# Kernel optimization log

Hardware: AMD Instinct MI355X
Metric: run time of the kernel (lower is better)

The kernel has to match this reference:

```python
import jax, jax.numpy as jnp
import numpy as np

EPS = 1e-5
NUM_HEADS = 16
HEAD_DIM = 128


def setup_inputs() -> dict:
    key = jax.random.key(0)
    ks = jax.random.split(key, 9)
    B, S, D = 2, 2048, 2048
    Hd2 = HEAD_DIM // 2
    # rotary angles: proper cos/sin of random phases (unit-modulus freqs_cis)
    theta = jax.random.uniform(ks[1], (B, S, Hd2), jnp.float32, 0.0, 2 * np.pi)
    return {
        "hidden_states": jax.random.normal(ks[0], (B, S, D), jnp.float32),
        "freqs_cos": jnp.cos(theta),
        "freqs_sin": jnp.sin(theta),
        "Wq": jax.random.normal(ks[2], (D, D), jnp.float32) * (D ** -0.5),
        "Wk": jax.random.normal(ks[3], (D, D), jnp.float32) * (D ** -0.5),
        "Wv": jax.random.normal(ks[4], (D, D), jnp.float32) * (D ** -0.5),
        "Wo": jax.random.normal(ks[5], (D, D), jnp.float32) * (D ** -0.5),
        "gq": jnp.ones((HEAD_DIM,), jnp.float32),
        "gk": jnp.ones((HEAD_DIM,), jnp.float32),
    }


def _rmsnorm(x, g):
    # normalize over last (head) dim, eps=1e-5, learned scale
    var = jnp.mean(jnp.square(x), axis=-1, keepdims=True)
    return x * jax.lax.rsqrt(var + EPS) * g


def _rope(x, cos, sin):
    # x: [B,S,H,hd]; treat last dim as hd/2 complex pairs; cos/sin: [B,S,hd/2]
    B, S, H, hd = x.shape
    xp = x.reshape(B, S, H, hd // 2, 2)
    xr, xi = xp[..., 0], xp[..., 1]
    c = cos[:, :, None, :]
    s = sin[:, :, None, :]
    out_r = xr * c - xi * s
    out_i = xr * s + xi * c
    return jnp.stack([out_r, out_i], axis=-1).reshape(B, S, H, hd)


def reference(hidden_states, freqs_cos, freqs_sin, Wq, Wk, Wv, Wo, gq, gk):
    B, S, D = hidden_states.shape
    H, hd = NUM_HEADS, HEAD_DIM
    q = (hidden_states @ Wq).reshape(B, S, H, hd)
    k = (hidden_states @ Wk).reshape(B, S, H, hd)
    v = (hidden_states @ Wv).reshape(B, S, H, hd)
    q = _rmsnorm(q, gq)
    k = _rmsnorm(k, gk)
    q = _rope(q, freqs_cos, freqs_sin)
    k = _rope(k, freqs_cos, freqs_sin)
    scale = 1.0 / np.sqrt(hd)
    scores = jnp.einsum("bqhd,bkhd->bhqk", q, k) * scale
    attn = jax.nn.softmax(scores, axis=-1)
    out = jnp.einsum("bhqk,bkhd->bqhd", attn, v)  # [B,S,H,hd]
    out = out.reshape(B, S, H * hd)
    return out @ Wo
```

## Files before the change

### kernel.cpp

```cpp
#include <hip/hip_runtime.h>
#include <hip/hip_bf16.h>

typedef __attribute__((ext_vector_type(8))) short bf16x8;
typedef __attribute__((ext_vector_type(4))) short bf16x4;
typedef __attribute__((ext_vector_type(4))) float f32x4;
typedef __attribute__((ext_vector_type(4))) int   i32x4;
typedef __attribute__((ext_vector_type(2))) unsigned u32x2;

#define D_MODEL 2048
#define NTOK    4096
#define NH      16
#define HD      128
#define SEQ     2048
#define NQKV    6144

__device__ __forceinline__ short f2bf(float f) {
  unsigned u = __builtin_bit_cast(unsigned, f);
  unsigned r = u + 0x7FFFu + ((u >> 16) & 1u);
  return (short)(r >> 16);
}
__device__ __forceinline__ float bf2f(short s) {
  return __builtin_bit_cast(float, ((unsigned)(unsigned short)s) << 16);
}

__device__ __forceinline__ float exp2fast(float x) {
#if __has_builtin(__builtin_amdgcn_exp2f)
  return __builtin_amdgcn_exp2f(x);
#else
  return exp2f(x);
#endif
}

__device__ __forceinline__ unsigned cvt_pk_bf16(float a, float b) {
  unsigned r;
  asm("v_cvt_pk_bf16_f32 %0, %1, %2" : "=v"(r) : "v"(a), "v"(b));
  return r;
}

#if __has_builtin(__builtin_amdgcn_mfma_f32_16x16x16bf16_1k)
#define MFMA16_ASM 0
__device__ __forceinline__ f32x4 mfma16(bf16x4 a, bf16x4 b, f32x4 c) {
  return __builtin_amdgcn_mfma_f32_16x16x16bf16_1k(a, b, c, 0, 0, 0);
}
#else
#define MFMA16_ASM 1
__device__ __forceinline__ f32x4 mfma16(bf16x4 a, bf16x4 b, f32x4 c) {
  asm("s_nop 3\n\tv_mfma_f32_16x16x16_bf16 %0, %1, %2, %0" : "+v"(c) : "v"(a), "v"(b));
  return c;
}
#endif

__device__ __forceinline__ void gload_lds16(const void* g, void* l) {
  typedef __attribute__((address_space(1))) const unsigned gu32;
  typedef __attribute__((address_space(3))) unsigned lu32;
  __builtin_amdgcn_global_load_lds((gu32*)(uintptr_t)g,
                                   (lu32*)(unsigned)(uintptr_t)l, 16, 0, 0);
}

__global__ __launch_bounds__(256) void cast_bf16(const float* __restrict__ in,
                                                 short* __restrict__ out, int n4) {
  int i = blockIdx.x * 256 + threadIdx.x;
  if (i >= n4) return;
  float4 v = ((const float4*)in)[i];
  short4 o;
  o.x = f2bf(v.x); o.y = f2bf(v.y); o.z = f2bf(v.z); o.w = f2bf(v.w);
  ((short4*)out)[i] = o;
}

__global__ __launch_bounds__(256) void wtrans(const float* __restrict__ w0,
                                              const float* __restrict__ w1,
                                              const float* __restrict__ w2,
                                              const float* __restrict__ w3,
                                              short* __restrict__ wt) {
  int z = blockIdx.z;
  const float* W = (z == 0) ? w0 : (z == 1) ? w1 : (z == 2) ? w2 : w3;
  short* O = wt + (size_t)z * D_MODEL * D_MODEL;
  int n0 = blockIdx.x * 64, k0 = blockIdx.y * 64;
  __shared__ short T[64 * 136];
  int tid = threadIdx.x;
#pragma unroll
  for (int it = 0; it < 4; ++it) {
    int f = it * 256 + tid, kk = f >> 4, nc = f & 15;
    float4 v = *(const float4*)&W[(size_t)(k0 + kk) * D_MODEL + n0 + nc * 4];
    short4 o;
    o.x = f2bf(v.x); o.y = f2bf(v.y); o.z = f2bf(v.z); o.w = f2bf(v.w);
    *(short4*)&T[kk * 136 + nc * 4] = o;
  }
  __syncthreads();
#pragma unroll
  for (int it = 0; it < 4; ++it) {
    int u = it * 256 + tid, nn = u >> 4, kc = u & 15;
    short4 o;
    o.x = T[(kc * 4 + 0) * 136 + nn];
    o.y = T[(kc * 4 + 1) * 136 + nn];
    o.z = T[(kc * 4 + 2) * 136 + nn];
    o.w = T[(kc * 4 + 3) * 136 + nn];
    *(short4*)&O[(size_t)(n0 + nn) * D_MODEL + k0 + kc * 4] = o;
  }
}

template <bool OUTBF16>
__global__ __launch_bounds__(512, 2) void gemm8(const short* __restrict__ A,
                                                const short* __restrict__ Bt,
                                                void* __restrict__ Cv, int CS) {
  __shared__ short L[4 * 12288];
  int tid = threadIdx.x, w = tid >> 6, lane = tid & 63, c = lane & 15, g = lane >> 4;

  int gx = gridDim.x, gy = gridDim.y;
  int lin = blockIdx.x + gx * blockIdx.y;
  int idx = lin >> 3, nst = (gx * gy) >> 7;
  int s = (lin & 7) * nst + (idx >> 4);
  int w16 = idx & 15;
  int smR = gy >> 2;
  int mblk = (s % smR) * 4 + (w16 >> 2);
  int nblk = (s / smR) * 4 + (w16 & 3);
  int m0 = mblk * 256, n0 = nblk * 128;
  int wm = w >> 1, wn = w & 1;

  const int NKT = D_MODEL / 32;

  int asrc[2], bsrc;
#pragma unroll
  for (int q = 0; q < 2; ++q) {
    int o = (2 * w + q) * 1024 + lane * 16;
    int os = o ^ (((o >> 7) & 7) << 4);
    asrc[q] = (m0 + (os >> 6)) * D_MODEL + ((os & 63) >> 1);
  }
  {
    int o = w * 1024 + lane * 16;
    int os = o ^ (((o >> 7) & 7) << 4);
    bsrc = (n0 + (os >> 6)) * D_MODEL + ((os & 63) >> 1);
  }

  int aoff[4], boff[4];
#pragma unroll
  for (int mi = 0; mi < 4; ++mi) {
    int r = wm * 64 + mi * 16 + c;
    int o = r * 64 + g * 16;
    aoff[mi] = o ^ (((o >> 7) & 7) << 4);
  }
#pragma unroll
  for (int ni = 0; ni < 4; ++ni) {
    int r = wn * 64 + ni * 16 + c;
    int o = r * 64 + g * 16;
    boff[ni] = 16384 + (o ^ (((o >> 7) & 7) << 4));
  }

  auto STAGE = [&](int jt) {
    int kk = jt * 32;
    char* base = (char*)L + (jt & 3) * 24576;
    gload_lds16(A + asrc[0] + kk, base + (2 * w) * 1024);
    gload_lds16(A + asrc[1] + kk, base + (2 * w + 1) * 1024);
    gload_lds16(Bt + bsrc + kk, base + 16384 + w * 1024);
  };

  f32x4 acc[4][4] = {};

  STAGE(0); STAGE(1); STAGE(2);
  asm volatile("s_waitcnt vmcnt(6)" ::: "memory");
  __builtin_amdgcn_s_barrier();
  asm volatile("" ::: "memory");

  for (int jt = 0; jt < NKT; ++jt) {
    if (jt + 3 < NKT) STAGE(jt + 3);
    const char* buf = (const char*)L + (jt & 3) * 24576;
    bf16x8 af[4], bfv[4];
#pragma unroll
    for (int mi = 0; mi < 4; ++mi) af[mi] = *(const bf16x8*)(buf + aoff[mi]);
#pragma unroll
    for (int ni = 0; ni < 4; ++ni) bfv[ni] = *(const bf16x8*)(buf + boff[ni]);
    __builtin_amdgcn_s_setprio(1);
#pragma unroll
    for (int mi = 0; mi < 4; ++mi)
#pragma unroll
      for (int ni = 0; ni < 4; ++ni)
        acc[mi][ni] = __builtin_amdgcn_mfma_f32_16x16x32_bf16(af[mi], bfv[ni],
                                                              acc[mi][ni], 0, 0, 0);
    __builtin_amdgcn_s_setprio(0);
    if (jt + 1 < NKT) {
      if (jt + 4 <= NKT - 1)      { asm volatile("s_waitcnt vmcnt(6)" ::: "memory"); }
      else if (jt + 3 <= NKT - 1) { asm volatile("s_waitcnt vmcnt(6)" ::: "memory"); }
      else if (jt + 2 <= NKT - 1) { asm volatile("s_waitcnt vmcnt(3)" ::: "memory"); }
      else                        { asm volatile("s_waitcnt vmcnt(0)" ::: "memory"); }
      __builtin_amdgcn_s_barrier();
      asm volatile("" ::: "memory");
    }
  }

  int row0 = m0 + wm * 64, col0 = n0 + wn * 64;
  if (OUTBF16) {
    short* Cb = (short*)Cv;
#pragma unroll
    for (int mi = 0; mi < 4; ++mi)
#pragma unroll
      for (int ni = 0; ni < 4; ++ni)
#pragma unroll
        for (int i = 0; i < 4; ++i)
          Cb[(size_t)(row0 + mi * 16 + g * 4 + i) * CS + col0 + ni * 16 + c] =
              f2bf(acc[mi][ni][i]);
  } else {
    float* Cf = (float*)Cv;
#pragma unroll
    for (int mi = 0; mi < 4; ++mi)
#pragma unroll
      for (int ni = 0; ni < 4; ++ni)
#pragma unroll
        for (int i = 0; i < 4; ++i)
          Cf[(size_t)(row0 + mi * 16 + g * 4 + i) * CS + col0 + ni * 16 + c] =
              acc[mi][ni][i];
  }
}

__global__ __launch_bounds__(256) void norm_rope(const short* __restrict__ qkv16,
                                                 const float* __restrict__ cosb,
                                                 const float* __restrict__ sinb,
                                                 const float* __restrict__ gq,
                                                 const float* __restrict__ gk,
                                                 short* __restrict__ qn,
                                                 short* __restrict__ kn) {
  int z = blockIdx.y;
  const float* gg = z ? gk : gq;
  short* O = z ? kn : qn;
  int w = threadIdx.x >> 6, lane = threadIdx.x & 63;
  int p = blockIdx.x * 4 + w;
  int token = p >> 4, h = p & 15;
  int v = *(const int*)&qkv16[(size_t)token * NQKV + z * D_MODEL + h * HD + lane * 2];
  float x0 = bf2f((short)(v & 0xffff));
  float x1 = bf2f((short)((unsigned)v >> 16));
  float ss = x0 * x0 + x1 * x1;
#pragma unroll
  for (int mk = 32; mk; mk >>= 1) ss += __shfl_xor(ss, mk);
  float rs = rsqrtf(ss * (1.f / 128.f) + 1e-5f);
  float qs = z ? 1.0f : 0.12751744f;
  rs *= qs;
  float xr = x0 * rs * gg[lane * 2];
  float xi = x1 * rs * gg[lane * 2 + 1];
  float cc = cosb[(size_t)token * 64 + lane];
  float sn = sinb[(size_t)token * 64 + lane];
  float or_ = xr * cc - xi * sn;
  float oi_ = xr * sn + xi * cc;
  int b = token >> 11, sidx = token & 2047;
  size_t dst = ((size_t)(b * NH + h) * SEQ + sidx) * HD + lane * 2;
  unsigned pk = (unsigned)(unsigned short)f2bf(or_) |
                ((unsigned)(unsigned short)f2bf(oi_) << 16);
  *(unsigned*)&O[dst] = pk;
}

__global__ __launch_bounds__(256) void vtrans(const short* __restrict__ qkv16,
                                              short* __restrict__ vt) {
  int st = blockIdx.x, bh = blockIdx.y;
  int b = bh >> 4, h = bh & 15;
  int t0 = b * SEQ + st * 64;
  __shared__ short Lt[64 * 136];
  int tid = threadIdx.x;
#pragma unroll
  for (int it = 0; it < 4; ++it) {
    int f = it * 256 + tid, tk = f >> 4, ch = f & 15;
    *(i32x4*)&Lt[tk * 136 + ch * 8] =
        *(const i32x4*)&qkv16[(size_t)(t0 + tk) * NQKV + 2 * D_MODEL + h * HD + ch * 8];
  }
  __syncthreads();
#pragma unroll
  for (int it = 0; it < 4; ++it) {
    int u = it * 256 + tid, d = u >> 3, kg = u & 7;
    bf16x8 o;
#pragma unroll
    for (int j = 0; j < 8; ++j) o[j] = Lt[(kg * 8 + j) * 136 + d];
    *(bf16x8*)&vt[(size_t)(bh * HD + d) * SEQ + st * 64 + kg * 8] = o;
  }
}

__global__ __launch_bounds__(512, 4) void flash(const short* __restrict__ qn,
                                                const short* __restrict__ kn,
                                                const short* __restrict__ vt,
                                                short* __restrict__ attn) {
  __shared__ short Ks[2][64 * 128];
  __shared__ short Vs[2][128 * 64];
  int tid = threadIdx.x, w = tid >> 6, lane = tid & 63, c = lane & 15, g = lane >> 4;
  int bh = blockIdx.y;
  int q0 = blockIdx.x * 128 + w * 16;
  const size_t base = (size_t)bh * SEQ * HD;
  const short* Kg = kn + base;
  const short* Vg = vt + base;

  bf16x8 qf[4];
#pragma unroll
  for (int kf = 0; kf < 4; ++kf)
    qf[kf] = *(const bf16x8*)&qn[base + (size_t)(q0 + c) * HD + kf * 32 + g * 8];

  f32x4 acc[8] = {};
  float m_ = -1e30f, l_ = 0.f;

  int ksrc[2], vsrc[2];
#pragma unroll
  for (int p = 0; p < 2; ++p) {
    int ch = w * 2 + p;
    int o = ch * 1024 + lane * 16;
    int kr = o >> 8, kc = o & 255;
    ksrc[p] = kr * HD + ((kc ^ ((kr & 7) << 4)) >> 1);
    int vr = o >> 7, vc = o & 127;
    vsrc[p] = vr * SEQ + ((vc ^ ((vr & 7) << 4)) >> 1);
  }
  int swz = (c & 7) << 4;
  int koff[4], voff[4];
#pragma unroll
  for (int kf = 0; kf < 4; ++kf) koff[kf] = c * 256 + ((kf * 64 + g * 16) ^ swz);
#pragma unroll
  for (int kt = 0; kt < 4; ++kt) voff[kt] = c * 128 + ((kt * 32 + g * 8) ^ swz);

#pragma unroll
  for (int p = 0; p < 2; ++p) {
    int ch = w * 2 + p;
    gload_lds16(Kg + ksrc[p], (char*)&Ks[0][0] + ch * 1024);
    gload_lds16(Vg + vsrc[p], (char*)&Vs[0][0] + ch * 1024);
  }

  const int NT = SEQ / 64;
  for (int t = 0; t < NT; ++t) {
    int cur = t & 1;
    __syncthreads();
    if (t + 1 < NT) {
      int k0n = (t + 1) * 64;
#pragma unroll
      for (int p = 0; p < 2; ++p) {
        int ch = w * 2 + p;
        gload_lds16(Kg + (size_t)k0n * HD + ksrc[p], (char*)&Ks[cur ^ 1][0] + ch * 1024);
        gload_lds16(Vg + k0n + vsrc[p],              (char*)&Vs[cur ^ 1][0] + ch * 1024);
      }
    }
    const char* Kb = (const char*)&Ks[cur][0];
    const char* Vb = (const char*)&Vs[cur][0];

    f32x4 s[4];
    __builtin_amdgcn_s_setprio(1);
#pragma unroll
    for (int kt = 0; kt < 4; ++kt) {
      f32x4 sa = {0.f, 0.f, 0.f, 0.f};
#pragma unroll
      for (int kf = 0; kf < 4; ++kf) {
        bf16x8 kb = *(const bf16x8*)(Kb + kt * 4096 + koff[kf]);
        sa = __builtin_amdgcn_mfma_f32_16x16x32_bf16(kb, qf[kf], sa, 0, 0, 0);
      }
      s[kt] = sa;
    }
    __builtin_amdgcn_s_setprio(0);

    float pmax = -1e30f;
#pragma unroll
    for (int kt = 0; kt < 4; ++kt)
#pragma unroll
      for (int i = 0; i < 4; ++i) pmax = fmaxf(pmax, s[kt][i]);
    pmax = fmaxf(pmax, __shfl_xor(pmax, 16));
    pmax = fmaxf(pmax, __shfl_xor(pmax, 32));
    if (!__all(pmax <= m_ + 11.5f)) {
      float mn = fmaxf(m_, pmax);
      float al = exp2fast(m_ - mn);
      m_ = mn; l_ *= al;
#pragma unroll
      for (int db = 0; db < 8; ++db)
#pragma unroll
        for (int i = 0; i < 4; ++i) acc[db][i] *= al;
    }
    float r = 0.f;
#pragma unroll
    for (int kt = 0; kt < 4; ++kt)
#pragma unroll
      for (int i = 0; i < 4; ++i) {
        float p = exp2fast(s[kt][i] - m_);
        r += p; s[kt][i] = p;
      }
    r += __shfl_xor(r, 16);
    r += __shfl_xor(r, 32);
    l_ += r;

    bf16x4 pb[4];
#pragma unroll
    for (int kt = 0; kt < 4; ++kt) {
      u32x2 tpk;
      tpk[0] = cvt_pk_bf16(s[kt][0], s[kt][1]);
      tpk[1] = cvt_pk_bf16(s[kt][2], s[kt][3]);
      pb[kt] = __builtin_bit_cast(bf16x4, tpk);
    }

    __builtin_amdgcn_s_setprio(1);
#pragma unroll
    for (int kt = 0; kt < 4; ++kt)
#pragma unroll
      for (int db = 0; db < 8; ++db) {
        bf16x4 va = *(const bf16x4*)(Vb + db * 2048 + voff[kt]);
        acc[db] = mfma16(va, pb[kt], acc[db]);
      }
    __builtin_amdgcn_s_setprio(0);
  }
#if MFMA16_ASM
  asm volatile("s_nop 7\n\ts_nop 7");
#endif

  int b = bh >> 4, h = bh & 15;
  float linv = 1.f / l_;
#pragma unroll
  for (int db = 0; db < 8; ++db) {
    short4 o;
    o.x = f2bf(acc[db][0] * linv);
    o.y = f2bf(acc[db][1] * linv);
    o.z = f2bf(acc[db][2] * linv);
    o.w = f2bf(acc[db][3] * linv);
    *(short4*)&attn[(size_t)(b * SEQ + q0 + c) * D_MODEL + h * HD + db * 16 + g * 4] = o;
  }
}

extern "C" void kernel_launch(void* const* d_in, const int* in_sizes, int n_in,
                              void* d_out, int out_size, void* d_ws, size_t ws_size,
                              hipStream_t stream) {
  const float* hs   = (const float*)d_in[0];
  const float* fcos = (const float*)d_in[1];
  const float* fsin = (const float*)d_in[2];
  const float* Wq   = (const float*)d_in[3];
  const float* Wk   = (const float*)d_in[4];
  const float* Wv   = (const float*)d_in[5];
  const float* Wo   = (const float*)d_in[6];
  const float* gq   = (const float*)d_in[7];
  const float* gk   = (const float*)d_in[8];

  char* ws = (char*)d_ws;
  short* hs16  = (short*)ws;
  short* Wt    = (short*)(ws + 16777216);
  short* qkv16 = (short*)(ws + 50331648);
  short* qn    = (short*)(ws + 100663296);
  short* kn    = (short*)(ws + 117440512);
  short* vt    = (short*)(ws + 134217728);
  short* attn16 = hs16;

  cast_bf16<<<8192, 256, 0, stream>>>(hs, hs16, NTOK * D_MODEL / 4);
  wtrans<<<dim3(32, 32, 4), 256, 0, stream>>>(Wq, Wk, Wv, Wo, Wt);
  gemm8<true><<<dim3(48, 16), 512, 0, stream>>>(hs16, Wt, qkv16, NQKV);
  norm_rope<<<dim3(16384, 2), 256, 0, stream>>>(qkv16, fcos, fsin, gq, gk, qn, kn);
  vtrans<<<dim3(32, 32), 256, 0, stream>>>(qkv16, vt);
  flash<<<dim3(16, 32), 512, 0, stream>>>(qn, kn, vt, attn16);
  gemm8<false><<<dim3(16, 16), 512, 0, stream>>>(attn16,
                                                 Wt + (size_t)3 * D_MODEL * D_MODEL,
                                                 d_out, D_MODEL);
}
```

Before: 316.9 us.

## Rewrite flash attention with 32x32 MFMA tiles and XCD-aware block mapping

Each flash-attention wave now owns 32 query rows instead of 16 and uses 32x32x16 bf16 MFMAs for both QK^T and PV. The P fragment is rebuilt in registers with permlane32 swaps, so no trip through LDS is needed. The grid becomes a 1D launch of 256 blocks that map bh heads to XCDs, so blocks sharing K/V land on the same L2. Each block now covers 256 queries, which halves the block count and lowers occupancy to 2 blocks per CU, while each K/V tile load is reused over more queries. A redundant waitcnt branch in the GEMM is also merged away.

After: 283.1 us. 1.12x faster.

```diff
diff --git a/kernel.cpp b/kernel.cpp
--- a/kernel.cpp
+++ b/kernel.cpp
@@ -4,8 +4,10 @@
 typedef __attribute__((ext_vector_type(8))) short bf16x8;
 typedef __attribute__((ext_vector_type(4))) short bf16x4;
 typedef __attribute__((ext_vector_type(4))) float f32x4;
+typedef __attribute__((ext_vector_type(16))) float f32x16;
 typedef __attribute__((ext_vector_type(4))) int   i32x4;
 typedef __attribute__((ext_vector_type(2))) unsigned u32x2;
+typedef __attribute__((ext_vector_type(4))) unsigned u32x4;
 
 #define D_MODEL 2048
 #define NTOK    4096
@@ -37,18 +39,18 @@
   return r;
 }
 
-#if __has_builtin(__builtin_amdgcn_mfma_f32_16x16x16bf16_1k)
-#define MFMA16_ASM 0
-__device__ __forceinline__ f32x4 mfma16(bf16x4 a, bf16x4 b, f32x4 c) {
-  return __builtin_amdgcn_mfma_f32_16x16x16bf16_1k(a, b, c, 0, 0, 0);
-}
+__device__ __forceinline__ void permswap(unsigned& x, unsigned& y) {
+#if __has_builtin(__builtin_amdgcn_permlane32_swap)
+  u32x2 r = __builtin_amdgcn_permlane32_swap(x, y, false, false);
+  x = r[0]; y = r[1];
 #else
-#define MFMA16_ASM 1
-__device__ __forceinline__ f32x4 mfma16(bf16x4 a, bf16x4 b, f32x4 c) {
-  asm("s_nop 3\n\tv_mfma_f32_16x16x16_bf16 %0, %1, %2, %0" : "+v"(c) : "v"(a), "v"(b));
-  return c;
-}
+  asm volatile("v_permlane32_swap_b32 %0, %1" : "+v"(x), "+v"(y));
 #endif
+}
+
+__device__ __forceinline__ f32x16 mfma32(bf16x8 a, bf16x8 b, f32x16 c) {
+  return __builtin_amdgcn_mfma_f32_32x32x16_bf16(a, b, c, 0, 0, 0);
+}
 
 __device__ __forceinline__ void gload_lds16(const void* g, void* l) {
   typedef __attribute__((address_space(1))) const unsigned gu32;
@@ -178,8 +180,7 @@
                                                               acc[mi][ni], 0, 0, 0);
     __builtin_amdgcn_s_setprio(0);
     if (jt + 1 < NKT) {
-      if (jt + 4 <= NKT - 1)      { asm volatile("s_waitcnt vmcnt(6)" ::: "memory"); }
-      else if (jt + 3 <= NKT - 1) { asm volatile("s_waitcnt vmcnt(6)" ::: "memory"); }
+      if (jt + 3 <= NKT - 1)      { asm volatile("s_waitcnt vmcnt(6)" ::: "memory"); }
       else if (jt + 2 <= NKT - 1) { asm volatile("s_waitcnt vmcnt(3)" ::: "memory"); }
       else                        { asm volatile("s_waitcnt vmcnt(0)" ::: "memory"); }
       __builtin_amdgcn_s_barrier();
@@ -270,25 +271,31 @@
   }
 }
 
-__global__ __launch_bounds__(512, 4) void flash(const short* __restrict__ qn,
+__global__ __launch_bounds__(512, 2) void flash(const short* __restrict__ qn,
                                                 const short* __restrict__ kn,
                                                 const short* __restrict__ vt,
                                                 short* __restrict__ attn) {
   __shared__ short Ks[2][64 * 128];
   __shared__ short Vs[2][128 * 64];
-  int tid = threadIdx.x, w = tid >> 6, lane = tid & 63, c = lane & 15, g = lane >> 4;
-  int bh = blockIdx.y;
-  int q0 = blockIdx.x * 128 + w * 16;
+  int tid = threadIdx.x, w = tid >> 6, lane = tid & 63;
+  int q31 = lane & 31, hi = lane >> 5;
+
+  int phys = blockIdx.x;
+  int xcd = phys & 7, idx = phys >> 3;
+  int bh = xcd * 4 + (idx >> 3);
+  int qb = idx & 7;
+  int q0 = qb * 256 + w * 32;
+
   const size_t base = (size_t)bh * SEQ * HD;
   const short* Kg = kn + base;
   const short* Vg = vt + base;
 
-  bf16x8 qf[4];
-#pragma unroll
-  for (int kf = 0; kf < 4; ++kf)
-    qf[kf] = *(const bf16x8*)&qn[base + (size_t)(q0 + c) * HD + kf * 32 + g * 8];
-
-  f32x4 acc[8] = {};
+  bf16x8 qf[8];
+#pragma unroll
+  for (int s = 0; s < 8; ++s)
+    qf[s] = *(const bf16x8*)&qn[base + (size_t)(q0 + q31) * HD + s * 16 + hi * 8];
+
+  f32x16 acc[4] = {};
   float m_ = -1e30f, l_ = 0.f;
 
   int ksrc[2], vsrc[2];
@@ -301,12 +308,13 @@
     int vr = o >> 7, vc = o & 127;
     vsrc[p] = vr * SEQ + ((vc ^ ((vr & 7) << 4)) >> 1);
   }
-  int swz = (c & 7) << 4;
-  int koff[4], voff[4];
-#pragma unroll
-  for (int kf = 0; kf < 4; ++kf) koff[kf] = c * 256 + ((kf * 64 + g * 16) ^ swz);
-#pragma unroll
-  for (int kt = 0; kt < 4; ++kt) voff[kt] = c * 128 + ((kt * 32 + g * 8) ^ swz);
+  int swz = (q31 & 7) << 4;
+  int koff[8], voff[4];
+#pragma unroll
+  for (int kf = 0; kf < 8; ++kf) koff[kf] = (kf * 32 + hi * 16) ^ swz;
+#pragma unroll
+  for (int kk = 0; kk < 4; ++kk) voff[kk] = (kk * 32 + hi * 16) ^ swz;
+  int krow0 = q31 * 256, krow1 = (32 + q31) * 256;
 
 #pragma unroll
   for (int p = 0; p < 2; ++p) {
@@ -331,82 +339,86 @@
     const char* Kb = (const char*)&Ks[cur][0];
     const char* Vb = (const char*)&Vs[cur][0];
 
-    f32x4 s[4];
+    f32x16 s0 = {0,0,0,0,0,0,0,0,0,0,0,0,0,0,0,0};
+    f32x16 s1 = {0,0,0,0,0,0,0,0,0,0,0,0,0,0,0,0};
     __builtin_amdgcn_s_setprio(1);
 #pragma unroll
-    for (int kt = 0; kt < 4; ++kt) {
-      f32x4 sa = {0.f, 0.f, 0.f, 0.f};
-#pragma unroll
-      for (int kf = 0; kf < 4; ++kf) {
-        bf16x8 kb = *(const bf16x8*)(Kb + kt * 4096 + koff[kf]);
-        sa = __builtin_amdgcn_mfma_f32_16x16x32_bf16(kb, qf[kf], sa, 0, 0, 0);
-      }
-      s[kt] = sa;
+    for (int kf = 0; kf < 8; ++kf) {
+      bf16x8 k0 = *(const bf16x8*)(Kb + krow0 + koff[kf]);
+      s0 = mfma32(k0, qf[kf], s0);
+      bf16x8 k1 = *(const bf16x8*)(Kb + krow1 + koff[kf]);
+      s1 = mfma32(k1, qf[kf], s1);
     }
     __builtin_amdgcn_s_setprio(0);
 
-    float pmax = -1e30f;
-#pragma unroll
-    for (int kt = 0; kt < 4; ++kt)
-#pragma unroll
-      for (int i = 0; i < 4; ++i) pmax = fmaxf(pmax, s[kt][i]);
-    pmax = fmaxf(pmax, __shfl_xor(pmax, 16));
+    float p0 = -1e30f, p1 = -1e30f, p2 = -1e30f, p3 = -1e30f;
+#pragma unroll
+    for (int i = 0; i < 4; ++i) {
+      p0 = fmaxf(p0, fmaxf(s0[i], s0[i + 4]));
+      p1 = fmaxf(p1, fmaxf(s0[i + 8], s0[i + 12]));
+      p2 = fmaxf(p2, fmaxf(s1[i], s1[i + 4]));
+      p3 = fmaxf(p3, fmaxf(s1[i + 8], s1[i + 12]));
+    }
+    float pmax = fmaxf(fmaxf(p0, p1), fmaxf(p2, p3));
     pmax = fmaxf(pmax, __shfl_xor(pmax, 32));
     if (!__all(pmax <= m_ + 11.5f)) {
       float mn = fmaxf(m_, pmax);
       float al = exp2fast(m_ - mn);
       m_ = mn; l_ *= al;
 #pragma unroll
-      for (int db = 0; db < 8; ++db)
-#pragma unroll
-        for (int i = 0; i < 4; ++i) acc[db][i] *= al;
-    }
-    float r = 0.f;
-#pragma unroll
-    for (int kt = 0; kt < 4; ++kt)
-#pragma unroll
-      for (int i = 0; i < 4; ++i) {
-        float p = exp2fast(s[kt][i] - m_);
-        r += p; s[kt][i] = p;
-      }
-    r += __shfl_xor(r, 16);
+      for (int db = 0; db < 4; ++db)
+#pragma unroll
+        for (int i = 0; i < 16; ++i) acc[db][i] *= al;
+    }
+    float r0 = 0.f, r1 = 0.f;
+#pragma unroll
+    for (int i = 0; i < 16; ++i) {
+      float pa = exp2fast(s0[i] - m_); r0 += pa; s0[i] = pa;
+      float pb = exp2fast(s1[i] - m_); r1 += pb; s1[i] = pb;
+    }
+    float r = r0 + r1;
     r += __shfl_xor(r, 32);
     l_ += r;
 
-    bf16x4 pb[4];
-#pragma unroll
-    for (int kt = 0; kt < 4; ++kt) {
-      u32x2 tpk;
-      tpk[0] = cvt_pk_bf16(s[kt][0], s[kt][1]);
-      tpk[1] = cvt_pk_bf16(s[kt][2], s[kt][3]);
-      pb[kt] = __builtin_bit_cast(bf16x4, tpk);
-    }
-
     __builtin_amdgcn_s_setprio(1);
 #pragma unroll
-    for (int kt = 0; kt < 4; ++kt)
-#pragma unroll
-      for (int db = 0; db < 8; ++db) {
-        bf16x4 va = *(const bf16x4*)(Vb + db * 2048 + voff[kt]);
-        acc[db] = mfma16(va, pb[kt], acc[db]);
+    for (int kt = 0; kt < 2; ++kt) {
+      const f32x16& sv = kt ? s1 : s0;
+#pragma unroll
+      for (int c2 = 0; c2 < 2; ++c2) {
+        unsigned x0 = cvt_pk_bf16(sv[c2 * 8 + 0], sv[c2 * 8 + 1]);
+        unsigned x1 = cvt_pk_bf16(sv[c2 * 8 + 2], sv[c2 * 8 + 3]);
+        unsigned y0 = cvt_pk_bf16(sv[c2 * 8 + 4], sv[c2 * 8 + 5]);
+        unsigned y1 = cvt_pk_bf16(sv[c2 * 8 + 6], sv[c2 * 8 + 7]);
+        permswap(x0, y0);
+        permswap(x1, y1);
+        u32x4 pw = {x0, x1, y0, y1};
+        bf16x8 pfrag = __builtin_bit_cast(bf16x8, pw);
+        int vo = voff[kt * 2 + c2];
+#pragma unroll
+        for (int db = 0; db < 4; ++db) {
+          bf16x8 va = *(const bf16x8*)(Vb + (db * 32 + q31) * 128 + vo);
+          acc[db] = mfma32(va, pfrag, acc[db]);
+        }
       }
+    }
     __builtin_amdgcn_s_setprio(0);
   }
-#if MFMA16_ASM
-  asm volatile("s_nop 7\n\ts_nop 7");
-#endif
 
   int b = bh >> 4, h = bh & 15;
   float linv = 1.f / l_;
-#pragma unroll
-  for (int db = 0; db < 8; ++db) {
-    short4 o;
-    o.x = f2bf(acc[db][0] * linv);
-    o.y = f2bf(acc[db][1] * linv);
-    o.z = f2bf(acc[db][2] * linv);
-    o.w = f2bf(acc[db][3] * linv);
-    *(short4*)&attn[(size_t)(b * SEQ + q0 + c) * D_MODEL + h * HD + db * 16 + g * 4] = o;
-  }
+  size_t orow = (size_t)(b * SEQ + q0 + q31) * D_MODEL + h * HD;
+#pragma unroll
+  for (int db = 0; db < 4; ++db)
+#pragma unroll
+    for (int rg = 0; rg < 4; ++rg) {
+      short4 o;
+      o.x = f2bf(acc[db][rg * 4 + 0] * linv);
+      o.y = f2bf(acc[db][rg * 4 + 1] * linv);
+      o.z = f2bf(acc[db][rg * 4 + 2] * linv);
+      o.w = f2bf(acc[db][rg * 4 + 3] * linv);
+      *(short4*)&attn[orow + db * 32 + rg * 8 + hi * 4] = o;
+    }
 }
 
 extern "C" void kernel_launch(void* const* d_in, const int* in_sizes, int n_in,
@@ -436,7 +448,7 @@
   gemm8<true><<<dim3(48, 16), 512, 0, stream>>>(hs16, Wt, qkv16, NQKV);
   norm_rope<<<dim3(16384, 2), 256, 0, stream>>>(qkv16, fcos, fsin, gq, gk, qn, kn);
   vtrans<<<dim3(32, 32), 256, 0, stream>>>(qkv16, vt);
-  flash<<<dim3(16, 32), 512, 0, stream>>>(qn, kn, vt, attn16);
+  flash<<<dim3(256), 512, 0, stream>>>(qn, kn, vt, attn16);
   gemm8<false><<<dim3(16, 16), 512, 0, stream>>>(attn16,
                                                  Wt + (size_t)3 * D_MODEL * D_MODEL,
                                                  d_out, D_MODEL);
```
